# Kernel optimization log

Measured on AMD Instinct MI355X. Metric: run time of the kernel, lower is better.

The kernel has to match this reference:

```python
import jax, jax.numpy as jnp
import numpy as np

D_MODEL = 1024
D_OUT = 64


def setup_inputs() -> dict:
    key = jax.random.key(0)
    ks = jax.random.split(key, 9)
    B, S = 4, 4096
    query = jax.random.normal(ks[0], (B, S, D_MODEL), dtype=jnp.float32)
    key_in = jax.random.normal(ks[1], (B, S, D_MODEL), dtype=jnp.float32)
    value = jax.random.normal(ks[2], (B, S, D_MODEL), dtype=jnp.float32)
    s = 1.0 / np.sqrt(D_MODEL)
    Wq = jax.random.uniform(ks[3], (D_MODEL, D_OUT), jnp.float32, -s, s)
    bq = jax.random.uniform(ks[4], (D_OUT,), jnp.float32, -s, s)
    Wk = jax.random.uniform(ks[5], (D_MODEL, D_OUT), jnp.float32, -s, s)
    bk = jax.random.uniform(ks[6], (D_OUT,), jnp.float32, -s, s)
    Wv = jax.random.uniform(ks[7], (D_MODEL, D_OUT), jnp.float32, -s, s)
    bv = jax.random.uniform(ks[8], (D_OUT,), jnp.float32, -s, s)
    return {"query": query, "key": key_in, "value": value,
            "Wq": Wq, "bq": bq, "Wk": Wk, "bk": bk, "Wv": Wv, "bv": bv}


def reference(query, key, value, Wq, bq, Wk, bk, Wv, bv):
    # Linear projections: [B,S,d_model] @ [d_model,d_out] + bias
    q = jnp.einsum('bsd,de->bse', query, Wq) + bq
    k = jnp.einsum('bsd,de->bse', key, Wk) + bk
    v = jnp.einsum('bsd,de->bse', value, Wv) + bv
    dim_k = k.shape[-1]
    # Full [B,S,S] score matrix (faithful to the unfused original)
    scores = jnp.einsum('bqe,bke->bqk', q, k) / jnp.sqrt(jnp.float32(dim_k))
    weights = jax.nn.softmax(scores, axis=-1)
    # dropout is identity in eval/inference mode
    out = jnp.einsum('bqk,bke->bqe', weights, v)
    return out
```

## Files before the change

kernel.cpp:

```cpp
#include <hip/hip_runtime.h>
#include <stdint.h>


typedef __attribute__((ext_vector_type(8))) short bf16x8;
typedef __attribute__((ext_vector_type(4))) float f32x4;

#define LOG2E_OVER8 0.1803368801111204f

#define GLOAD16(gptr, lptr)                                                            \
  __builtin_amdgcn_global_load_lds((const __attribute__((address_space(1))) uint32_t*)(gptr), \
                                   (__attribute__((address_space(3))) uint32_t*)(lptr), 16, 0, 0)

__device__ __forceinline__ unsigned short f2bf(float f) {
  union { float f; uint32_t u; } v; v.f = f;
  return (unsigned short)((v.u + 0x7FFFu + ((v.u >> 16) & 1u)) >> 16);
}
__device__ __forceinline__ uint32_t f2bf2(float a, float b) {
  return (uint32_t)f2bf(a) | ((uint32_t)f2bf(b) << 16);
}
__device__ __forceinline__ unsigned short f2bf_fast(float f) {
  union { float f; uint32_t u; } v; v.f = f;
  return (unsigned short)((v.u + 0x8000u) >> 16);
}

__global__ void prep_kernel(const float* __restrict__ Wq, const float* __restrict__ bq,
                            const float* __restrict__ Wk, const float* __restrict__ bk,
                            const float* __restrict__ Wv, const float* __restrict__ bv,
                            unsigned short* __restrict__ wt, float* __restrict__ bias) {
  int idx = blockIdx.x * 256 + threadIdx.x;
  int p = idx >> 16;
  int rem = idx & 65535;
  int k = rem >> 6, col = rem & 63;
  const float* W = p == 0 ? Wq : (p == 1 ? Wk : Wv);
  float scale = (p == 0) ? LOG2E_OVER8 : 1.0f;
  wt[(p << 16) + col * 1024 + k] = f2bf(W[rem] * scale);
  if (idx < 192) {
    int pp = idx >> 6, cc = idx & 63;
    const float* bsrc = pp == 0 ? bq : (pp == 1 ? bk : bv);
    bias[idx] = bsrc[cc] * ((pp == 0) ? LOG2E_OVER8 : 1.0f);
  }
}

__global__ __launch_bounds__(256)
void proj_kernel(const float* __restrict__ Xq, const float* __restrict__ Xk,
                 const float* __restrict__ Xv,
                 const unsigned short* __restrict__ wt, const float* __restrict__ bias,
                 unsigned short* __restrict__ qo, unsigned short* __restrict__ ko,
                 unsigned short* __restrict__ vo) {
  __shared__ float Xs[2][64][64];
  __shared__ unsigned short Wsh[2][64][64];
  const int p = blockIdx.y;
  const float* X = p == 0 ? Xq : (p == 1 ? Xk : Xv);
  const int row0 = blockIdx.x * 64;
  const int tid = threadIdx.x;
  const int lane = tid & 63, wv = tid >> 6, c = lane & 15, G = lane >> 4;
  const int wvoff = wv * 1024;

  const int xsrow = tid >> 4;
  const int xcol = ((tid & 15) ^ xsrow) * 4;
  const int wcolr = tid >> 3;
  const int wkoff = ((tid & 7) ^ (wcolr & 7)) * 8;

  f32x4 acc[4] = {};

  auto STAGE = [&](int bufi, int kk) {
    char* xb = (char*)&Xs[bufi][0][0];
    char* wb = (char*)&Wsh[bufi][0][0];
#pragma unroll
    for (int s = 0; s < 4; s++) {
      const float* src = X + (size_t)(row0 + s * 16 + xsrow) * 1024 + kk + xcol;
      GLOAD16(src, xb + s * 4096 + wvoff);
    }
#pragma unroll
    for (int s2 = 0; s2 < 2; s2++) {
      const unsigned short* src = wt + (p << 16) + (size_t)(s2 * 32 + wcolr) * 1024 + kk + wkoff;
      GLOAD16(src, wb + s2 * 4096 + wvoff);
    }
  };

  STAGE(0, 0);
  __syncthreads();
  int buf = 0;
  for (int kk = 0; kk < 1024; kk += 64) {
    if (kk < 960) STAGE(buf ^ 1, kk + 64);
    const char* xb = (const char*)&Xs[buf][0][0];
    const char* wb = (const char*)&Wsh[buf][0][0];
#pragma unroll
    for (int k2 = 0; k2 < 2; k2++) {
      float4 f0 = *(const float4*)(xb + (wv * 16 + c) * 256 + ((k2 * 8 + G * 2) ^ c) * 16);
      float4 f1 = *(const float4*)(xb + (wv * 16 + c) * 256 + ((k2 * 8 + G * 2 + 1) ^ c) * 16);
      union { uint32_t u[4]; bf16x8 v; } cv;
      cv.u[0] = f2bf2(f0.x, f0.y); cv.u[1] = f2bf2(f0.z, f0.w);
      cv.u[2] = f2bf2(f1.x, f1.y); cv.u[3] = f2bf2(f1.z, f1.w);
      bf16x8 a = cv.v;
#pragma unroll
      for (int n = 0; n < 4; n++) {
        bf16x8 bw = *(const bf16x8*)(wb + (16 * n + c) * 128 + (((k2 * 4 + G) ^ (c & 7)) * 16));
        acc[n] = __builtin_amdgcn_mfma_f32_16x16x32_bf16(a, bw, acc[n], 0, 0, 0);
      }
    }
    __syncthreads();
    buf ^= 1;
  }

  float bcol[4];
#pragma unroll
  for (int n = 0; n < 4; n++) bcol[n] = bias[p * 64 + 16 * n + c];
  if (p < 2) {
    unsigned short* out = (p == 0) ? qo : ko;
#pragma unroll
    for (int n = 0; n < 4; n++)
#pragma unroll
      for (int r = 0; r < 4; r++) {
        int row = row0 + wv * 16 + G * 4 + r;
        out[(size_t)row * 64 + 16 * n + c] = f2bf(acc[n][r] + bcol[n]);
      }
  } else {
#pragma unroll
    for (int n = 0; n < 4; n++)
#pragma unroll
      for (int r = 0; r < 4; r++) {
        int row = row0 + wv * 16 + G * 4 + r;
        int bb = row >> 12, sl = row & 4095;
        int e = 16 * n + c;
        vo[((size_t)(bb * 64 + e) << 12) + sl] = f2bf(acc[n][r] + bcol[n]);
      }
  }
}

__global__ __launch_bounds__(256)
void attn_kernel(const unsigned short* __restrict__ q_ws, const unsigned short* __restrict__ k_ws,
                 const unsigned short* __restrict__ vt_ws, float* __restrict__ out) {
  __shared__ unsigned short Ks[2][2][64][64];
  __shared__ unsigned short Vs[2][2][64][64];
  __shared__ uint32_t Pl[4][16][36];
  __shared__ float msh[2][16], lsh[2][16];
  const int bid = blockIdx.x;
  const int b = (bid & 7) >> 1;
  const int xt = ((bid >> 3) << 1) | (bid & 1);
  const int tid = threadIdx.x;
  const int lane = tid & 63, wv = tid >> 6, c = lane & 15, G = lane >> 4;
  const int ws_ = wv & 1, g = wv >> 1;
  const int qrow = xt * 32 + ws_ * 16;
  const int wvoff = wv * 1024;

  const int srow = tid >> 3;
  const int scol = ((tid & 7) ^ (srow & 7)) * 8;

  bf16x8 aq[2];
#pragma unroll
  for (int k2 = 0; k2 < 2; k2++)
    aq[k2] = *(const bf16x8*)(q_ws + ((size_t)(b * 4096 + qrow + c) << 6) + k2 * 32 + G * 8);

  f32x4 o[4] = {};
  float mr[4] = {-1e30f, -1e30f, -1e30f, -1e30f};
  float lp[4] = {};

  auto STAGE = [&](int bufi, int t) {
#pragma unroll
    for (int gb = 0; gb < 2; gb++) {
      int kv0 = gb * 2048 + t * 64;
      char* kb = (char*)&Ks[bufi][gb][0][0];
      char* vb = (char*)&Vs[bufi][gb][0][0];
#pragma unroll
      for (int h = 0; h < 2; h++) {
        const unsigned short* ksrc = k_ws + ((size_t)(b * 4096 + kv0 + h * 32 + srow) << 6) + scol;
        GLOAD16(ksrc, kb + h * 4096 + wvoff);
        const unsigned short* vsrc = vt_ws + ((size_t)(b * 64 + h * 32 + srow) << 12) + kv0 + scol;
        GLOAD16(vsrc, vb + h * 4096 + wvoff);
      }
    }
  };

  STAGE(0, 0);
  __syncthreads();
  int buf = 0;
  for (int t = 0; t < 32; t++) {
    if (t < 31) STAGE(buf ^ 1, t + 1);
    const char* kb = (const char*)&Ks[buf][g][0][0];
    const char* vb = (const char*)&Vs[buf][g][0][0];

    f32x4 sc[4] = {};
#pragma unroll
    for (int k2 = 0; k2 < 2; k2++)
#pragma unroll
      for (int f = 0; f < 4; f++) {
        bf16x8 bk = *(const bf16x8*)(kb + (16 * f + c) * 128 + (((k2 * 4 + G) ^ (c & 7)) * 16));
        sc[f] = __builtin_amdgcn_mfma_f32_16x16x32_bf16(aq[k2], bk, sc[f], 0, 0, 0);
      }

    float mn[4];
#pragma unroll
    for (int r = 0; r < 4; r++)
      mn[r] = fmaxf(fmaxf(sc[0][r], sc[1][r]), fmaxf(sc[2][r], sc[3][r]));
#pragma unroll
    for (int msk = 1; msk <= 8; msk <<= 1)
#pragma unroll
      for (int r = 0; r < 4; r++)
        mn[r] = fmaxf(mn[r], __shfl_xor(mn[r], msk));

    float pv[4][4];
#pragma unroll
    for (int r = 0; r < 4; r++) {
      float M = fmaxf(mr[r], mn[r]);
      float al = __builtin_amdgcn_exp2f(mr[r] - M);
      mr[r] = M;
      lp[r] *= al;
#pragma unroll
      for (int df = 0; df < 4; df++) o[df][r] *= al;
#pragma unroll
      for (int f = 0; f < 4; f++) pv[f][r] = __builtin_amdgcn_exp2f(sc[f][r] - M);
      lp[r] += (pv[0][r] + pv[1][r]) + (pv[2][r] + pv[3][r]);
    }

    unsigned short* plw = (unsigned short*)&Pl[wv][0][0];
#pragma unroll
    for (int f = 0; f < 4; f++)
#pragma unroll
      for (int r = 0; r < 4; r++)
        plw[(4 * G + r) * 72 + 16 * f + c] = f2bf_fast(pv[f][r]);

    bf16x8 pa[2];
    pa[0] = *(const bf16x8*)((const char*)&Pl[wv][0][0] + c * 144 + G * 16);
    pa[1] = *(const bf16x8*)((const char*)&Pl[wv][0][0] + c * 144 + 64 + G * 16);
#pragma unroll
    for (int k2 = 0; k2 < 2; k2++)
#pragma unroll
      for (int df = 0; df < 4; df++) {
        bf16x8 bvv = *(const bf16x8*)(vb + (16 * df + c) * 128 + (((k2 * 4 + G) ^ (c & 7)) * 16));
        o[df] = __builtin_amdgcn_mfma_f32_16x16x32_bf16(pa[k2], bvv, o[df], 0, 0, 0);
      }
    __syncthreads();
    buf ^= 1;
  }

#pragma unroll
  for (int msk = 1; msk <= 8; msk <<= 1)
#pragma unroll
    for (int r = 0; r < 4; r++) lp[r] += __shfl_xor(lp[r], msk);

  float* Osh = (float*)&Ks[0][0][0][0];
  if (g == 1) {
#pragma unroll
    for (int df = 0; df < 4; df++)
#pragma unroll
      for (int r = 0; r < 4; r++)
        Osh[(ws_ * 16 + 4 * G + r) * 65 + 16 * df + c] = o[df][r];
    if (c == 0) {
#pragma unroll
      for (int r = 0; r < 4; r++) {
        msh[ws_][4 * G + r] = mr[r];
        lsh[ws_][4 * G + r] = lp[r];
      }
    }
  }
  __syncthreads();
  if (g == 0) {
#pragma unroll
    for (int r = 0; r < 4; r++) {
      int rowi = 4 * G + r;
      float m1 = msh[ws_][rowi], l1 = lsh[ws_][rowi];
      float M = fmaxf(mr[r], m1);
      float a0 = __builtin_amdgcn_exp2f(mr[r] - M);
      float a1 = __builtin_amdgcn_exp2f(m1 - M);
      float inv = 1.0f / (a0 * lp[r] + a1 * l1);
#pragma unroll
      for (int df = 0; df < 4; df++) {
        float val = (a0 * o[df][r] + a1 * Osh[(ws_ * 16 + rowi) * 65 + 16 * df + c]) * inv;
        out[((size_t)(b * 4096 + qrow + rowi) << 6) + 16 * df + c] = val;
      }
    }
  }
}

extern "C" void kernel_launch(void* const* d_in, const int* in_sizes, int n_in,
                              void* d_out, int out_size, void* d_ws, size_t ws_size,
                              hipStream_t stream) {
  const float* query = (const float*)d_in[0];
  const float* key   = (const float*)d_in[1];
  const float* value = (const float*)d_in[2];
  const float* Wq = (const float*)d_in[3];
  const float* bq = (const float*)d_in[4];
  const float* Wk = (const float*)d_in[5];
  const float* bk = (const float*)d_in[6];
  const float* Wv = (const float*)d_in[7];
  const float* bv = (const float*)d_in[8];

  char* ws = (char*)d_ws;
  unsigned short* q_ws  = (unsigned short*)(ws);
  unsigned short* k_ws  = (unsigned short*)(ws + (2u << 20));
  unsigned short* vt_ws = (unsigned short*)(ws + (4u << 20));
  unsigned short* wt_ws = (unsigned short*)(ws + (6u << 20));
  float* bias_ws        = (float*)(ws + (6u << 20) + 393216);

  prep_kernel<<<768, 256, 0, stream>>>(Wq, bq, Wk, bk, Wv, bv, wt_ws, bias_ws);
  proj_kernel<<<dim3(256, 3), 256, 0, stream>>>(query, key, value, wt_ws, bias_ws,
                                                q_ws, k_ws, vt_ws);
  attn_kernel<<<512, 256, 0, stream>>>(q_ws, k_ws, vt_ws, (float*)d_out);
}
```

Before: 286.3 us.

## Preload full weight tile into LDS and stream X directly to registers

The projection kernel now loads the whole 64x1024 bf16 weight slice for its projection into LDS once per block. Each wave streams its fp32 X rows straight from global memory into registers with a 3-deep software prefetch, which removes the per-step LDS staging of X and the per-iteration barriers. Blocks grow to 512 threads covering 128 rows, and the 128 KB LDS footprint limits occupancy. The attention kernel also raises wave priority around its MFMA sections with s_setprio.

```diff
diff --git a/kernel.cpp b/kernel.cpp
--- a/kernel.cpp
+++ b/kernel.cpp
@@ -41,71 +41,74 @@
   }
 }
 
-__global__ __launch_bounds__(256)
+__global__ __launch_bounds__(512)
 void proj_kernel(const float* __restrict__ Xq, const float* __restrict__ Xk,
                  const float* __restrict__ Xv,
                  const unsigned short* __restrict__ wt, const float* __restrict__ bias,
                  unsigned short* __restrict__ qo, unsigned short* __restrict__ ko,
                  unsigned short* __restrict__ vo) {
-  __shared__ float Xs[2][64][64];
-  __shared__ unsigned short Wsh[2][64][64];
+  __shared__ unsigned short Wlds[16][64][64];
   const int p = blockIdx.y;
   const float* X = p == 0 ? Xq : (p == 1 ? Xk : Xv);
-  const int row0 = blockIdx.x * 64;
+  const int row0 = blockIdx.x * 128;
   const int tid = threadIdx.x;
-  const int lane = tid & 63, wv = tid >> 6, c = lane & 15, G = lane >> 4;
-  const int wvoff = wv * 1024;
-
-  const int xsrow = tid >> 4;
-  const int xcol = ((tid & 15) ^ xsrow) * 4;
-  const int wcolr = tid >> 3;
-  const int wkoff = ((tid & 7) ^ (wcolr & 7)) * 8;
+  const int lane = tid & 63, wv = tid >> 6, cc = lane & 15, G = lane >> 4;
+
+  {
+    char* wl = (char*)&Wlds[0][0][0];
+#pragma unroll
+    for (int c2 = 0; c2 < 2; c2++) {
+      int ch = wv * 2 + c2;
+#pragma unroll
+      for (int i = 0; i < 8; i++) {
+        int r = i * 8 + (lane >> 3);
+        int s = lane & 7;
+        const unsigned short* src = wt + (p << 16) + r * 1024 + ch * 64 + ((s ^ (r & 7)) << 3);
+        GLOAD16(src, wl + ch * 8192 + i * 1024);
+      }
+    }
+  }
+  __syncthreads();
+
+  const float* xrow = X + (size_t)(row0 + wv * 16 + cc) * 1024;
+  const char* wl = (const char*)&Wlds[0][0][0];
 
   f32x4 acc[4] = {};
-
-  auto STAGE = [&](int bufi, int kk) {
-    char* xb = (char*)&Xs[bufi][0][0];
-    char* wb = (char*)&Wsh[bufi][0][0];
-#pragma unroll
-    for (int s = 0; s < 4; s++) {
-      const float* src = X + (size_t)(row0 + s * 16 + xsrow) * 1024 + kk + xcol;
-      GLOAD16(src, xb + s * 4096 + wvoff);
-    }
-#pragma unroll
-    for (int s2 = 0; s2 < 2; s2++) {
-      const unsigned short* src = wt + (p << 16) + (size_t)(s2 * 32 + wcolr) * 1024 + kk + wkoff;
-      GLOAD16(src, wb + s2 * 4096 + wvoff);
-    }
-  };
-
-  STAGE(0, 0);
-  __syncthreads();
-  int buf = 0;
-  for (int kk = 0; kk < 1024; kk += 64) {
-    if (kk < 960) STAGE(buf ^ 1, kk + 64);
-    const char* xb = (const char*)&Xs[buf][0][0];
-    const char* wb = (const char*)&Wsh[buf][0][0];
+  float4 xf[3][4];
+
+#define LOADX(jj)                                                              \
+  {                                                                            \
+    const float4* s_ = (const float4*)(xrow + (jj) * 64);                      \
+    xf[(jj) % 3][0] = s_[G * 2];       xf[(jj) % 3][1] = s_[G * 2 + 1];        \
+    xf[(jj) % 3][2] = s_[8 + G * 2];   xf[(jj) % 3][3] = s_[8 + G * 2 + 1];    \
+  }
+
+  LOADX(0);
+  LOADX(1);
+#pragma unroll
+  for (int j = 0; j < 16; j++) {
+    if (j < 14) LOADX(j + 2);
 #pragma unroll
     for (int k2 = 0; k2 < 2; k2++) {
-      float4 f0 = *(const float4*)(xb + (wv * 16 + c) * 256 + ((k2 * 8 + G * 2) ^ c) * 16);
-      float4 f1 = *(const float4*)(xb + (wv * 16 + c) * 256 + ((k2 * 8 + G * 2 + 1) ^ c) * 16);
+      float4 p0 = xf[j % 3][k2 * 2];
+      float4 p1 = xf[j % 3][k2 * 2 + 1];
       union { uint32_t u[4]; bf16x8 v; } cv;
-      cv.u[0] = f2bf2(f0.x, f0.y); cv.u[1] = f2bf2(f0.z, f0.w);
-      cv.u[2] = f2bf2(f1.x, f1.y); cv.u[3] = f2bf2(f1.z, f1.w);
+      cv.u[0] = f2bf2(p0.x, p0.y); cv.u[1] = f2bf2(p0.z, p0.w);
+      cv.u[2] = f2bf2(p1.x, p1.y); cv.u[3] = f2bf2(p1.z, p1.w);
       bf16x8 a = cv.v;
 #pragma unroll
       for (int n = 0; n < 4; n++) {
-        bf16x8 bw = *(const bf16x8*)(wb + (16 * n + c) * 128 + (((k2 * 4 + G) ^ (c & 7)) * 16));
+        bf16x8 bw = *(const bf16x8*)(wl + j * 8192 + (16 * n + cc) * 128 +
+                                     (((k2 * 4 + G) ^ (cc & 7)) << 4));
         acc[n] = __builtin_amdgcn_mfma_f32_16x16x32_bf16(a, bw, acc[n], 0, 0, 0);
       }
     }
-    __syncthreads();
-    buf ^= 1;
-  }
+  }
+#undef LOADX
 
   float bcol[4];
 #pragma unroll
-  for (int n = 0; n < 4; n++) bcol[n] = bias[p * 64 + 16 * n + c];
+  for (int n = 0; n < 4; n++) bcol[n] = bias[p * 64 + 16 * n + cc];
   if (p < 2) {
     unsigned short* out = (p == 0) ? qo : ko;
 #pragma unroll
@@ -113,7 +116,7 @@
 #pragma unroll
       for (int r = 0; r < 4; r++) {
         int row = row0 + wv * 16 + G * 4 + r;
-        out[(size_t)row * 64 + 16 * n + c] = f2bf(acc[n][r] + bcol[n]);
+        out[(size_t)row * 64 + 16 * n + cc] = f2bf(acc[n][r] + bcol[n]);
       }
   } else {
 #pragma unroll
@@ -122,7 +125,7 @@
       for (int r = 0; r < 4; r++) {
         int row = row0 + wv * 16 + G * 4 + r;
         int bb = row >> 12, sl = row & 4095;
-        int e = 16 * n + c;
+        int e = 16 * n + cc;
         vo[((size_t)(bb * 64 + e) << 12) + sl] = f2bf(acc[n][r] + bcol[n]);
       }
   }
@@ -181,6 +184,7 @@
     const char* vb = (const char*)&Vs[buf][g][0][0];
 
     f32x4 sc[4] = {};
+    __builtin_amdgcn_s_setprio(1);
 #pragma unroll
     for (int k2 = 0; k2 < 2; k2++)
 #pragma unroll
@@ -188,6 +192,7 @@
         bf16x8 bk = *(const bf16x8*)(kb + (16 * f + c) * 128 + (((k2 * 4 + G) ^ (c & 7)) * 16));
         sc[f] = __builtin_amdgcn_mfma_f32_16x16x32_bf16(aq[k2], bk, sc[f], 0, 0, 0);
       }
+    __builtin_amdgcn_s_setprio(0);
 
     float mn[4];
 #pragma unroll
@@ -223,6 +228,7 @@
     bf16x8 pa[2];
     pa[0] = *(const bf16x8*)((const char*)&Pl[wv][0][0] + c * 144 + G * 16);
     pa[1] = *(const bf16x8*)((const char*)&Pl[wv][0][0] + c * 144 + 64 + G * 16);
+    __builtin_amdgcn_s_setprio(1);
 #pragma unroll
     for (int k2 = 0; k2 < 2; k2++)
 #pragma unroll
@@ -230,6 +236,7 @@
         bf16x8 bvv = *(const bf16x8*)(vb + (16 * df + c) * 128 + (((k2 * 4 + G) ^ (c & 7)) * 16));
         o[df] = __builtin_amdgcn_mfma_f32_16x16x32_bf16(pa[k2], bvv, o[df], 0, 0, 0);
       }
+    __builtin_amdgcn_s_setprio(0);
     __syncthreads();
     buf ^= 1;
   }
@@ -294,7 +301,7 @@
   float* bias_ws        = (float*)(ws + (6u << 20) + 393216);
 
   prep_kernel<<<768, 256, 0, stream>>>(Wq, bq, Wk, bk, Wv, bv, wt_ws, bias_ws);
-  proj_kernel<<<dim3(256, 3), 256, 0, stream>>>(query, key, value, wt_ws, bias_ws,
+  proj_kernel<<<dim3(128, 3), 512, 0, stream>>>(query, key, value, wt_ws, bias_ws,
                                                 q_ws, k_ws, vt_ws);
   attn_kernel<<<512, 256, 0, stream>>>(q_ws, k_ws, vt_ws, (float*)d_out);
 }
```

Measured after the change: 297.5 us. 1.04x slower.
